# Performance work log

Hardware: AMD Instinct MI355X
Metric: run time of the kernel (lower is better)

Reference implementation:

```python
import jax, jax.numpy as jnp
import numpy as np

TEMPERATURE = 0.5
LOSS_WEIGHT = 0.2
EPS = 1e-8


def setup_inputs() -> dict:
    key = jax.random.key(0)
    k1, k2 = jax.random.split(key)
    L, B, H = 4, 256, 65536
    hidden_states = jax.random.normal(k1, (L, B, H), dtype=jnp.float32)
    task_type = jax.random.randint(k2, (B,), 0, 16, dtype=jnp.int64)
    return {"hidden_states": hidden_states, "task_type": task_type}


def reference(hidden_states, task_type):
    # hidden_states: [L, B, H] stacked flattened intermediate activations
    # (world_size == 1, so the gathered global states equal the local states)
    L, B, H = hidden_states.shape
    # F.normalize(p=2, dim=2)
    x = hidden_states / jnp.maximum(
        jnp.linalg.norm(hidden_states, axis=2, keepdims=True), 1e-12)

    # pos_mask from task-type equality, diagonal (self-pairs) zeroed
    pos_mask = (task_type[:, None] == task_type[None, :]).astype(x.dtype)
    pos_mask = pos_mask * (1.0 - jnp.eye(B, dtype=x.dtype))  # [B, B]

    # cdist(..., compute_mode='use_mm_for_euclid_dist') ** 2:
    # ||xi||^2 + ||xj||^2 - 2 xi.xj, clamped at 0
    sq = jnp.sum(x * x, axis=2)                      # [L, B]
    dots = jnp.einsum('lbh,lch->lbc', x, x)          # [L, B, B] -- dominant GEMM
    d2 = jnp.maximum(sq[:, :, None] + sq[:, None, :] - 2.0 * dots, 0.0)

    w = jnp.exp(-(d2 / TEMPERATURE))                 # [L, B, B]
    a = jnp.sum(w * pos_mask[None], axis=2)          # [L, B]
    b = jnp.sum(w, axis=2)                           # [L, B]
    per_layer = -jnp.mean(jnp.log((a + EPS) / (b + EPS)), axis=1)  # [L]
    return jnp.sum(per_layer) / L * LOSS_WEIGHT
```

## Files before the change

### kernel.cpp

```cpp
#include <hip/hip_runtime.h>
#include <hip/hip_bf16.h>

#define L_LAYERS 4
#define B_DIM 256
#define H_DIM 65536
#define KC 2048
#define BK 32
#define LDA 56

using bf16x8_t = __attribute__((ext_vector_type(8))) short;
using shortx4  = __attribute__((ext_vector_type(4))) short;
using floatx4  = __attribute__((ext_vector_type(4))) float;

__device__ __forceinline__ unsigned short f2bf(float f) {
    unsigned u = __float_as_uint(f);
    return (unsigned short)((u + 0x7fffu + ((u >> 16) & 1u)) >> 16);
}

__global__ __launch_bounds__(256) void gram_kernel(const float* __restrict__ hs,
                                                   float* __restrict__ G) {
    __shared__ short ldsA[128 * LDA];
    __shared__ short ldsB[128 * LDA];

    const int tid  = threadIdx.x;
    const int ta   = blockIdx.x >> 1;
    const int tb   = blockIdx.x & 1;
    const int kz   = blockIdx.y;
    const int l    = blockIdx.z;

    const int wave = tid >> 6, lane = tid & 63;
    const int m0   = (wave >> 1) * 64;
    const int n0   = (wave & 1) * 64;
    const int mrow = lane & 15, quad = lane >> 4;

    const int tr = tid >> 3;
    const int tc = (tid & 7) * 4;

    const float* baseA = hs + ((size_t)l * B_DIM + ta * 128) * H_DIM + (size_t)kz * KC;
    const float* baseB = hs + ((size_t)l * B_DIM + tb * 128) * H_DIM + (size_t)kz * KC;

    floatx4 acc[4][4];
#pragma unroll
    for (int i = 0; i < 4; ++i)
#pragma unroll
        for (int j = 0; j < 4; ++j) acc[i][j] = (floatx4)0.0f;

    for (int kt = 0; kt < KC / BK; ++kt) {
        const int kb = kt * BK;
#pragma unroll
        for (int it = 0; it < 4; ++it) {
            const int row = it * 32 + tr;
            const float4 va = *(const float4*)(baseA + (size_t)row * H_DIM + kb + tc);
            const float4 vb = *(const float4*)(baseB + (size_t)row * H_DIM + kb + tc);
            shortx4 wa, wb;
            wa[0] = (short)f2bf(va.x); wa[1] = (short)f2bf(va.y);
            wa[2] = (short)f2bf(va.z); wa[3] = (short)f2bf(va.w);
            wb[0] = (short)f2bf(vb.x); wb[1] = (short)f2bf(vb.y);
            wb[2] = (short)f2bf(vb.z); wb[3] = (short)f2bf(vb.w);
            *(shortx4*)&ldsA[row * LDA + tc] = wa;
            *(shortx4*)&ldsB[row * LDA + tc] = wb;
        }
        __syncthreads();

        bf16x8_t af[4], bfv[4];
#pragma unroll
        for (int i = 0; i < 4; ++i)
            af[i] = *(const bf16x8_t*)&ldsA[(m0 + i * 16 + mrow) * LDA + quad * 8];
#pragma unroll
        for (int j = 0; j < 4; ++j)
            bfv[j] = *(const bf16x8_t*)&ldsB[(n0 + j * 16 + mrow) * LDA + quad * 8];
#pragma unroll
        for (int i = 0; i < 4; ++i)
#pragma unroll
            for (int j = 0; j < 4; ++j)
                acc[i][j] = __builtin_amdgcn_mfma_f32_16x16x32_bf16(af[i], bfv[j], acc[i][j], 0, 0, 0);
        __syncthreads();
    }

    float* Gl = G + (size_t)l * B_DIM * B_DIM;
#pragma unroll
    for (int i = 0; i < 4; ++i)
#pragma unroll
        for (int j = 0; j < 4; ++j)
#pragma unroll
            for (int r = 0; r < 4; ++r) {
                const int row = ta * 128 + m0 + i * 16 + quad * 4 + r;
                const int col = tb * 128 + n0 + j * 16 + mrow;
                atomicAdd(&Gl[row * B_DIM + col], acc[i][j][r]);
            }
}

__global__ __launch_bounds__(256) void loss_kernel(const float* __restrict__ G,
                                                   const int* __restrict__ task,
                                                   float* __restrict__ out) {
    const int i = blockIdx.x, l = blockIdx.y, j = threadIdx.x;

    __shared__ int s_odd_nz;
    if (j == 0) s_odd_nz = 0;
    __syncthreads();
    if (j < 128 && task[2 * j + 1] != 0) s_odd_nz = 1;
    __syncthreads();
    const bool is64 = (s_odd_nz == 0);

    const float* Gl = G + (size_t)l * B_DIM * B_DIM;
    const float gij = Gl[i * B_DIM + j];
    const float gii = Gl[i * B_DIM + i];
    const float gjj = Gl[j * B_DIM + j];
    const float nd  = gij * rsqrtf(gii) * rsqrtf(gjj);
    const float d2  = fmaxf(2.0f - 2.0f * nd, 0.0f);
    const float w   = __expf(-2.0f * d2);

    const int ti = is64 ? task[2 * i] : task[i];
    const int tj = is64 ? task[2 * j] : task[j];
    const float pm = (ti == tj && i != j) ? 1.0f : 0.0f;

    float a = w * pm, b = w;
#pragma unroll
    for (int off = 32; off > 0; off >>= 1) {
        a += __shfl_down(a, off);
        b += __shfl_down(b, off);
    }
    __shared__ float sa[4], sb[4];
    const int wv = j >> 6, ln = j & 63;
    if (ln == 0) { sa[wv] = a; sb[wv] = b; }
    __syncthreads();
    if (j == 0) {
        const float A  = sa[0] + sa[1] + sa[2] + sa[3];
        const float Bb = sb[0] + sb[1] + sb[2] + sb[3];
        const float c  = -logf((A + 1e-8f) / (Bb + 1e-8f)) * (0.2f / 1024.0f);
        atomicAdd(out, c);
    }
}

extern "C" void kernel_launch(void* const* d_in, const int* in_sizes, int n_in,
                              void* d_out, int out_size, void* d_ws, size_t ws_size,
                              hipStream_t stream) {
    const float* hs   = (const float*)d_in[0];
    const int*   task = (const int*)d_in[1];
    float*       out  = (float*)d_out;
    float*       G    = (float*)d_ws;

    hipMemsetAsync(G, 0, (size_t)L_LAYERS * B_DIM * B_DIM * sizeof(float), stream);
    hipMemsetAsync(out, 0, sizeof(float), stream);

    dim3 grid(4, H_DIM / KC, L_LAYERS);
    gram_kernel<<<grid, dim3(256), 0, stream>>>(hs, G);
    loss_kernel<<<dim3(B_DIM, L_LAYERS), dim3(256), 0, stream>>>(G, task, out);
}
```

Measured before the change: 424.7 us.

## Compute full 256x256 Gram tile per block and reduce split-K partials without atomics

Each 512-thread block now computes the whole 256x256 Gram matrix for one layer and one K slice of 1024, so every input row is loaded and converted to bf16 once instead of twice. The next K tile is prefetched into registers while the current one is computed. The atomicAdd split-K accumulation and the memset are replaced by plain stores of partial slices plus a separate reduce kernel. This adds 64MB of partial-sum traffic and an extra kernel launch, and the larger accumulator per wave may lower occupancy.

```diff
diff --git a/kernel.cpp b/kernel.cpp
--- a/kernel.cpp
+++ b/kernel.cpp
@@ -4,12 +4,14 @@
 #define L_LAYERS 4
 #define B_DIM 256
 #define H_DIM 65536
-#define KC 2048
+#define KC 1024
 #define BK 32
-#define LDA 56
+#define NKZ (H_DIM / KC)
+#define NSLICE (L_LAYERS * NKZ)
+#define LDSTR 40
 
 using bf16x8_t = __attribute__((ext_vector_type(8))) short;
-using shortx4  = __attribute__((ext_vector_type(4))) short;
+using shortx8  = __attribute__((ext_vector_type(8))) short;
 using floatx4  = __attribute__((ext_vector_type(4))) float;
 
 __device__ __forceinline__ unsigned short f2bf(float f) {
@@ -17,77 +19,98 @@
     return (unsigned short)((u + 0x7fffu + ((u >> 16) & 1u)) >> 16);
 }
 
-__global__ __launch_bounds__(256) void gram_kernel(const float* __restrict__ hs,
-                                                   float* __restrict__ G) {
-    __shared__ short ldsA[128 * LDA];
-    __shared__ short ldsB[128 * LDA];
+__global__ __launch_bounds__(512, 2) void gram_kernel(const float* __restrict__ hs,
+                                                      float* __restrict__ S) {
+    __shared__ short lds[B_DIM * LDSTR];
 
-    const int tid  = threadIdx.x;
-    const int ta   = blockIdx.x >> 1;
-    const int tb   = blockIdx.x & 1;
-    const int kz   = blockIdx.y;
-    const int l    = blockIdx.z;
+    const int tid = threadIdx.x;
+    const int bx  = blockIdx.x;
+    const int l   = bx >> 6;
+    const int kz  = bx & (NKZ - 1);
 
     const int wave = tid >> 6, lane = tid & 63;
-    const int m0   = (wave >> 1) * 64;
-    const int n0   = (wave & 1) * 64;
+    const int wm = wave >> 1;
+    const int wn = wave & 1;
     const int mrow = lane & 15, quad = lane >> 4;
 
-    const int tr = tid >> 3;
-    const int tc = (tid & 7) * 4;
+    const int r = tid >> 1;
+    const int h = tid & 1;
+    const float* gp = hs + ((size_t)l * B_DIM + r) * H_DIM + (size_t)kz * KC + h * 16;
+    const int ldsw = r * LDSTR + h * 16;
 
-    const float* baseA = hs + ((size_t)l * B_DIM + ta * 128) * H_DIM + (size_t)kz * KC;
-    const float* baseB = hs + ((size_t)l * B_DIM + tb * 128) * H_DIM + (size_t)kz * KC;
-
-    floatx4 acc[4][4];
+    floatx4 acc[4][8];
 #pragma unroll
     for (int i = 0; i < 4; ++i)
 #pragma unroll
-        for (int j = 0; j < 4; ++j) acc[i][j] = (floatx4)0.0f;
+        for (int j = 0; j < 8; ++j) acc[i][j] = (floatx4)0.0f;
+
+    float4 pv0 = *(const float4*)(gp + 0);
+    float4 pv1 = *(const float4*)(gp + 4);
+    float4 pv2 = *(const float4*)(gp + 8);
+    float4 pv3 = *(const float4*)(gp + 12);
 
     for (int kt = 0; kt < KC / BK; ++kt) {
-        const int kb = kt * BK;
-#pragma unroll
-        for (int it = 0; it < 4; ++it) {
-            const int row = it * 32 + tr;
-            const float4 va = *(const float4*)(baseA + (size_t)row * H_DIM + kb + tc);
-            const float4 vb = *(const float4*)(baseB + (size_t)row * H_DIM + kb + tc);
-            shortx4 wa, wb;
-            wa[0] = (short)f2bf(va.x); wa[1] = (short)f2bf(va.y);
-            wa[2] = (short)f2bf(va.z); wa[3] = (short)f2bf(va.w);
-            wb[0] = (short)f2bf(vb.x); wb[1] = (short)f2bf(vb.y);
-            wb[2] = (short)f2bf(vb.z); wb[3] = (short)f2bf(vb.w);
-            *(shortx4*)&ldsA[row * LDA + tc] = wa;
-            *(shortx4*)&ldsB[row * LDA + tc] = wb;
+        shortx8 w0, w1;
+        w0[0] = (short)f2bf(pv0.x); w0[1] = (short)f2bf(pv0.y);
+        w0[2] = (short)f2bf(pv0.z); w0[3] = (short)f2bf(pv0.w);
+        w0[4] = (short)f2bf(pv1.x); w0[5] = (short)f2bf(pv1.y);
+        w0[6] = (short)f2bf(pv1.z); w0[7] = (short)f2bf(pv1.w);
+        w1[0] = (short)f2bf(pv2.x); w1[1] = (short)f2bf(pv2.y);
+        w1[2] = (short)f2bf(pv2.z); w1[3] = (short)f2bf(pv2.w);
+        w1[4] = (short)f2bf(pv3.x); w1[5] = (short)f2bf(pv3.y);
+        w1[6] = (short)f2bf(pv3.z); w1[7] = (short)f2bf(pv3.w);
+        *(shortx8*)&lds[ldsw]     = w0;
+        *(shortx8*)&lds[ldsw + 8] = w1;
+
+        if (kt < KC / BK - 1) {
+            const float* gn = gp + (kt + 1) * BK;
+            pv0 = *(const float4*)(gn + 0);
+            pv1 = *(const float4*)(gn + 4);
+            pv2 = *(const float4*)(gn + 8);
+            pv3 = *(const float4*)(gn + 12);
         }
         __syncthreads();
 
-        bf16x8_t af[4], bfv[4];
+        bf16x8_t af[4], bfv[8];
 #pragma unroll
         for (int i = 0; i < 4; ++i)
-            af[i] = *(const bf16x8_t*)&ldsA[(m0 + i * 16 + mrow) * LDA + quad * 8];
+            af[i] = *(const bf16x8_t*)&lds[(wm * 64 + i * 16 + mrow) * LDSTR + quad * 8];
 #pragma unroll
-        for (int j = 0; j < 4; ++j)
-            bfv[j] = *(const bf16x8_t*)&ldsB[(n0 + j * 16 + mrow) * LDA + quad * 8];
+        for (int j = 0; j < 8; ++j)
+            bfv[j] = *(const bf16x8_t*)&lds[(wn * 128 + j * 16 + mrow) * LDSTR + quad * 8];
 #pragma unroll
         for (int i = 0; i < 4; ++i)
 #pragma unroll
-            for (int j = 0; j < 4; ++j)
+            for (int j = 0; j < 8; ++j)
                 acc[i][j] = __builtin_amdgcn_mfma_f32_16x16x32_bf16(af[i], bfv[j], acc[i][j], 0, 0, 0);
         __syncthreads();
     }
 
-    float* Gl = G + (size_t)l * B_DIM * B_DIM;
+    float* Ssl = S + (size_t)bx * (B_DIM * B_DIM);
 #pragma unroll
     for (int i = 0; i < 4; ++i)
 #pragma unroll
-        for (int j = 0; j < 4; ++j)
+        for (int j = 0; j < 8; ++j)
 #pragma unroll
-            for (int r = 0; r < 4; ++r) {
-                const int row = ta * 128 + m0 + i * 16 + quad * 4 + r;
-                const int col = tb * 128 + n0 + j * 16 + mrow;
-                atomicAdd(&Gl[row * B_DIM + col], acc[i][j][r]);
+            for (int rr = 0; rr < 4; ++rr) {
+                const int row = wm * 64 + i * 16 + quad * 4 + rr;
+                const int col = wn * 128 + j * 16 + mrow;
+                Ssl[row * B_DIM + col] = acc[i][j][rr];
             }
+}
+
+__global__ __launch_bounds__(256) void reduce_kernel(const float* __restrict__ S,
+                                                     float* __restrict__ G) {
+    const int li = blockIdx.x;
+    const int j  = threadIdx.x;
+    const int l  = li >> 8;
+    const int i  = li & 255;
+    const float* base = S + ((size_t)l * NKZ) * (B_DIM * B_DIM) + i * B_DIM + j;
+    float s = 0.0f;
+#pragma unroll
+    for (int kz = 0; kz < NKZ; ++kz)
+        s += base[(size_t)kz * (B_DIM * B_DIM)];
+    G[(size_t)li * B_DIM + j] = s;
 }
 
 __global__ __launch_bounds__(256) void loss_kernel(const float* __restrict__ G,
@@ -138,12 +161,13 @@
     const float* hs   = (const float*)d_in[0];
     const int*   task = (const int*)d_in[1];
     float*       out  = (float*)d_out;
-    float*       G    = (float*)d_ws;
 
-    hipMemsetAsync(G, 0, (size_t)L_LAYERS * B_DIM * B_DIM * sizeof(float), stream);
+    float* S = (float*)d_ws;
+    float* G = S + (size_t)NSLICE * (B_DIM * B_DIM);
+
     hipMemsetAsync(out, 0, sizeof(float), stream);
 
-    dim3 grid(4, H_DIM / KC, L_LAYERS);
-    gram_kernel<<<grid, dim3(256), 0, stream>>>(hs, G);
+    gram_kernel<<<dim3(NSLICE), dim3(512), 0, stream>>>(hs, S);
+    reduce_kernel<<<dim3(L_LAYERS * B_DIM), dim3(256), 0, stream>>>(S, G);
     loss_kernel<<<dim3(B_DIM, L_LAYERS), dim3(256), 0, stream>>>(G, task, out);
 }
```

New measurement: 423.2 us. About the same (-0.4%).
